# Kernel optimization log

Measured on AMD Instinct MI355X. Metric: run time of the kernel, lower is better.

## Reference

```python
import jax, jax.numpy as jnp
import numpy as np

N_HEADS = 16
D_MODEL = 1024
HEAD_DIM = D_MODEL // N_HEADS
B, S = 2, 2048


def setup_inputs() -> dict:
    key = jax.random.key(0)
    ks = jax.random.split(key, 10)
    scale = 1.0 / np.sqrt(D_MODEL)
    inp = {
        "query_tokens": jax.random.normal(ks[0], (B, S, D_MODEL), dtype=jnp.float32),
        "key_or_value_tokens": jax.random.normal(ks[1], (B, S, D_MODEL), dtype=jnp.float32),
        "mask": jnp.ones((B, S, S), dtype=jnp.int32),
        "Wq": jax.random.normal(ks[2], (D_MODEL, D_MODEL), dtype=jnp.float32) * scale,
        "bq": jnp.zeros((D_MODEL,), dtype=jnp.float32),
        "Wk": jax.random.normal(ks[3], (D_MODEL, D_MODEL), dtype=jnp.float32) * scale,
        "bk": jnp.zeros((D_MODEL,), dtype=jnp.float32),
        "Wv": jax.random.normal(ks[4], (D_MODEL, D_MODEL), dtype=jnp.float32) * scale,
        "bv": jnp.zeros((D_MODEL,), dtype=jnp.float32),
        "Wo": jax.random.normal(ks[5], (D_MODEL, D_MODEL), dtype=jnp.float32) * scale,
        "bo": jnp.zeros((D_MODEL,), dtype=jnp.float32),
    }
    return inp


def reference(query_tokens, key_or_value_tokens, mask, Wq, bq, Wk, bk, Wv, bv, Wo, bo):
    b, s, d = query_tokens.shape
    h, dh = N_HEADS, HEAD_DIM

    def proj(x, W, bias):
        # torch Linear: x @ W.T + b ; then split heads -> (b, h, s, dh)
        y = jnp.einsum("bsd,ed->bse", x, W) + bias
        return y.reshape(b, -1, h, dh).transpose(0, 2, 1, 3)

    q = proj(query_tokens, Wq, bq)
    k = proj(key_or_value_tokens, Wk, bk)
    v = proj(key_or_value_tokens, Wv, bv)

    scores = jnp.einsum("bhqd,bhkd->bhqk", q, k) / jnp.sqrt(jnp.float32(dh))
    # mask: (b, Sq, Sk) -> (b, 1, Sq, Sk); zeros get large negative fill
    scores = jnp.where(mask[:, None, :, :] == 0, jnp.float32(-1e9), scores)
    attn = jax.nn.softmax(scores, axis=-1)
    out = jnp.einsum("bhqk,bhkd->bhqd", attn, v)
    out = out.transpose(0, 2, 1, 3).reshape(b, s, d)
    return jnp.einsum("bsd,ed->bse", out, Wo) + bo
```

## Files before the change

### kernel.cpp

```cpp
#include <hip/hip_runtime.h>
#include <hip/hip_bf16.h>

typedef __bf16 bf16_8 __attribute__((ext_vector_type(8)));
typedef __bf16 bf16_4 __attribute__((ext_vector_type(4)));
typedef float  f32_4  __attribute__((ext_vector_type(4)));

#define NH 16
#define DHD 64
#define BB 2
#define SS 2048
#define DD 1024

__device__ __forceinline__ void gload16(const __bf16* g, __bf16* l) {
    __builtin_amdgcn_global_load_lds(
        (const __attribute__((address_space(1))) void*)g,
        (__attribute__((address_space(3))) void*)l, 16, 0, 0);
}

__global__ __launch_bounds__(256) void conv_all(
    const float* __restrict__ s0, const float* __restrict__ s1,
    const float* __restrict__ s2, const float* __restrict__ s3,
    const float* __restrict__ s4, const float* __restrict__ s5,
    __bf16* __restrict__ d0, __bf16* __restrict__ d1, __bf16* __restrict__ d2,
    __bf16* __restrict__ d3, __bf16* __restrict__ d4, __bf16* __restrict__ d5) {
    const int y = blockIdx.y;
    if (y >= 2 && blockIdx.x >= 1024) return;
    const float* s = (y == 0) ? s0 : (y == 1) ? s1 : (y == 2) ? s2
                   : (y == 3) ? s3 : (y == 4) ? s4 : s5;
    __bf16* d      = (y == 0) ? d0 : (y == 1) ? d1 : (y == 2) ? d2
                   : (y == 3) ? d3 : (y == 4) ? d4 : d5;
    const int i = (blockIdx.x * 256 + threadIdx.x) * 4;
    f32_4 v = *(const f32_4*)&s[i];
    bf16_4 o; o[0] = (__bf16)v[0]; o[1] = (__bf16)v[1];
    o[2] = (__bf16)v[2]; o[3] = (__bf16)v[3];
    *(bf16_4*)&d[i] = o;
}

__global__ __launch_bounds__(256) void mask_flags_k(const int* __restrict__ mask,
                                                    int* __restrict__ flags) {
    const int id = blockIdx.x;
    const int b = id >> 10, qt = (id >> 5) & 31, kt = id & 31;
    const int t = threadIdx.x;
    const int row = t >> 2, seg = t & 3;
    const int* p = mask + ((size_t)b * SS + qt * 64 + row) * SS + kt * 64 + seg * 16;
    int any0 = 0;
#pragma unroll
    for (int i = 0; i < 4; ++i) {
        int4 v = *(const int4*)&p[i * 4];
        any0 |= (v.x == 0) | (v.y == 0) | (v.z == 0) | (v.w == 0);
    }
    unsigned long long bal = __ballot(any0);
    __shared__ int sf[4];
    if ((t & 63) == 0) sf[t >> 6] = (bal != 0ULL);
    __syncthreads();
    if (t == 0) flags[id] = sf[0] | sf[1] | sf[2] | sf[3];
}

template <int LAYOUT>
__device__ __forceinline__ void gemm_body(const __bf16* __restrict__ A,
                                          const __bf16* __restrict__ W,
                                          const float* __restrict__ bias,
                                          __bf16* __restrict__ out,
                                          __bf16* ldsA, __bf16* ldsB) {
    const int tid  = threadIdx.x;
    const int lane = tid & 63;
    const int w    = tid >> 6;
    const int quad = lane >> 4;
    const int l15  = lane & 15;
    const int wm   = (w >> 1) * 64;
    const int wn   = (w & 1) * 64;
    const int m0   = blockIdx.x * 128;
    const int n0   = blockIdx.y * 128;

    f32_4 acc[4][4] = {};

    for (int kt = 0; kt < 1024; kt += 32) {
#pragma unroll
        for (int cc = 0; cc < 2; ++cc) {
            const int c   = tid + cc * 256;
            const int row = c >> 2;
            const int cp  = c & 3;
            gload16(&A[(size_t)(m0 + row) * 1024 + kt + cp * 8], &ldsA[c * 8]);
            gload16(&W[(size_t)(n0 + row) * 1024 + kt + cp * 8], &ldsB[c * 8]);
        }
        __syncthreads();

        bf16_8 af[4], bfr[4];
#pragma unroll
        for (int i = 0; i < 4; ++i)
            af[i] = *(const bf16_8*)&ldsA[(wm + i * 16 + l15) * 32 + quad * 8];
#pragma unroll
        for (int j = 0; j < 4; ++j)
            bfr[j] = *(const bf16_8*)&ldsB[(wn + j * 16 + l15) * 32 + quad * 8];
#pragma unroll
        for (int i = 0; i < 4; ++i)
#pragma unroll
            for (int j = 0; j < 4; ++j)
                acc[i][j] = __builtin_amdgcn_mfma_f32_16x16x32_bf16(
                    af[i], bfr[j], acc[i][j], 0, 0, 0);
        __syncthreads();
    }

#pragma unroll
    for (int i = 0; i < 4; ++i) {
#pragma unroll
        for (int j = 0; j < 4; ++j) {
            const int col = n0 + wn + j * 16 + l15;
            const float bv = bias[col];
            if (LAYOUT == 2) {
                const int row0 = m0 + wm + i * 16 + quad * 4;
                bf16_4 pk;
#pragma unroll
                for (int r = 0; r < 4; ++r) pk[r] = (__bf16)(acc[i][j][r] + bv);
                const int bb = row0 >> 11, s0 = row0 & 2047;
                const int h = col >> 6, dh = col & 63;
                *(bf16_4*)&out[(((size_t)bb * NH + h) * DHD + dh) * SS + s0] = pk;
            } else {
#pragma unroll
                for (int r = 0; r < 4; ++r) {
                    const int row = m0 + wm + i * 16 + quad * 4 + r;
                    out[(((size_t)(row >> 11) * NH + (col >> 6)) * SS +
                         (row & 2047)) * DHD + (col & 63)] =
                        (__bf16)(acc[i][j][r] + bv);
                }
            }
        }
    }
}

__global__ __launch_bounds__(256) void gemm_qkv(
    const __bf16* __restrict__ Xq, const __bf16* __restrict__ Xkv,
    const __bf16* __restrict__ Wq, const float* __restrict__ bq,
    const __bf16* __restrict__ Wk, const float* __restrict__ bk,
    const __bf16* __restrict__ Wv, const float* __restrict__ bv,
    __bf16* __restrict__ Qo, __bf16* __restrict__ Ko, __bf16* __restrict__ VTo) {
    __shared__ __align__(16) __bf16 ldsA[128 * 32];
    __shared__ __align__(16) __bf16 ldsB[128 * 32];
    const int z = blockIdx.z;
    const __bf16* A    = (z == 0) ? Xq : Xkv;
    const __bf16* W    = (z == 0) ? Wq : (z == 1 ? Wk : Wv);
    const float* bias  = (z == 0) ? bq : (z == 1 ? bk : bv);
    if (z == 2)
        gemm_body<2>(A, W, bias, VTo, ldsA, ldsB);
    else
        gemm_body<0>(A, W, bias, (z == 0) ? Qo : Ko, ldsA, ldsB);
}

__global__ __launch_bounds__(256) void gemm_final(
    const __bf16* __restrict__ A, const __bf16* __restrict__ W,
    const float* __restrict__ bias, float* __restrict__ out) {
    __shared__ __align__(16) __bf16 ldsA[64 * 32];
    __shared__ __align__(16) __bf16 ldsB[64 * 32];
    const int tid  = threadIdx.x;
    const int lane = tid & 63;
    const int w    = tid >> 6;
    const int quad = lane >> 4;
    const int l15  = lane & 15;
    const int wm   = (w >> 1) * 32;
    const int wn   = (w & 1) * 32;
    const int m0   = blockIdx.x * 64;
    const int n0   = blockIdx.y * 64;

    const int isB = w >> 1;
    const __bf16* src = isB ? W : A;
    const int     bN  = isB ? n0 : m0;
    __bf16*       dst = isB ? ldsB : ldsA;
    const int     w2  = w & 1;

    f32_4 acc[2][2] = {};

    for (int kt = 0; kt < 1024; kt += 32) {
#pragma unroll
        for (int cc = 0; cc < 2; ++cc) {
            const int c   = w2 * 128 + cc * 64 + lane;
            const int row = c >> 2;
            const int cp  = c & 3;
            gload16(&src[(size_t)(bN + row) * 1024 + kt + cp * 8], &dst[c * 8]);
        }
        __syncthreads();

        bf16_8 af[2], bfr[2];
#pragma unroll
        for (int i = 0; i < 2; ++i)
            af[i] = *(const bf16_8*)&ldsA[(wm + i * 16 + l15) * 32 + quad * 8];
#pragma unroll
        for (int j = 0; j < 2; ++j)
            bfr[j] = *(const bf16_8*)&ldsB[(wn + j * 16 + l15) * 32 + quad * 8];
#pragma unroll
        for (int i = 0; i < 2; ++i)
#pragma unroll
            for (int j = 0; j < 2; ++j)
                acc[i][j] = __builtin_amdgcn_mfma_f32_16x16x32_bf16(
                    af[i], bfr[j], acc[i][j], 0, 0, 0);
        __syncthreads();
    }

#pragma unroll
    for (int i = 0; i < 2; ++i)
#pragma unroll
        for (int j = 0; j < 2; ++j) {
            const int col = n0 + wn + j * 16 + l15;
            const float bv = bias[col];
#pragma unroll
            for (int r = 0; r < 4; ++r) {
                const int row = m0 + wm + i * 16 + quad * 4 + r;
                out[(size_t)row * 1024 + col] = acc[i][j][r] + bv;
            }
        }
}

__global__ __launch_bounds__(256) void flash_attn(
    const __bf16* __restrict__ Q, const __bf16* __restrict__ K,
    const __bf16* __restrict__ VT, const int* __restrict__ mask,
    const int* __restrict__ flags, __bf16* __restrict__ O) {
    __shared__ __align__(16) __bf16 ldsK[64 * 72];
    __shared__ __align__(16) __bf16 ldsVT[64 * 72];
    __shared__ __align__(16) __bf16 ldsP[64 * 72];

    const int tid  = threadIdx.x;
    const int lane = tid & 63;
    const int w    = tid >> 6;
    const int quad = lane >> 4;
    const int l15  = lane & 15;
    const int q0   = blockIdx.x * 64;
    const int bh   = blockIdx.y;
    const int b    = bh >> 4;

    const __bf16* Qb  = Q + (size_t)bh * SS * DHD;
    const __bf16* Kb  = K + (size_t)bh * SS * DHD;
    const __bf16* VTb = VT + (size_t)bh * DHD * SS;
    const int*    mb  = mask + (size_t)b * SS * SS;
    const int*    fl  = flags + ((size_t)b * 32 + blockIdx.x) * 32;

    bf16_8 qa[2];
#pragma unroll
    for (int ks = 0; ks < 2; ++ks) {
        bf16_8 t = *(const bf16_8*)&Qb[(size_t)(q0 + w * 16 + l15) * DHD + ks * 32 + quad * 8];
#pragma unroll
        for (int e = 0; e < 8; ++e)
            qa[ks][e] = (__bf16)((float)t[e] * 0.18033688011112042f);
    }

    f32_4 of[4] = {};
    float li[4] = {0.f, 0.f, 0.f, 0.f};

    const int rowA = tid >> 3,          cpA = tid & 7;
    const int rowB = (tid + 256) >> 3;

    uint4 kr0 = *(const uint4*)&Kb[(size_t)rowA * DHD + cpA * 8];
    uint4 kr1 = *(const uint4*)&Kb[(size_t)rowB * DHD + cpA * 8];
    uint4 vr0 = *(const uint4*)&VTb[(size_t)rowA * SS + cpA * 8];
    uint4 vr1 = *(const uint4*)&VTb[(size_t)rowB * SS + cpA * 8];

    for (int k0 = 0; k0 < SS; k0 += 64) {
        *(uint4*)&ldsK[rowA * 72 + cpA * 8]  = kr0;
        *(uint4*)&ldsK[rowB * 72 + cpA * 8]  = kr1;
        *(uint4*)&ldsVT[rowA * 72 + cpA * 8] = vr0;
        *(uint4*)&ldsVT[rowB * 72 + cpA * 8] = vr1;
        if (k0 + 64 < SS) {
            const int kn = k0 + 64;
            kr0 = *(const uint4*)&Kb[(size_t)(kn + rowA) * DHD + cpA * 8];
            kr1 = *(const uint4*)&Kb[(size_t)(kn + rowB) * DHD + cpA * 8];
            vr0 = *(const uint4*)&VTb[(size_t)rowA * SS + kn + cpA * 8];
            vr1 = *(const uint4*)&VTb[(size_t)rowB * SS + kn + cpA * 8];
        }
        __syncthreads();

        f32_4 sa[4] = {};
#pragma unroll
        for (int ks = 0; ks < 2; ++ks) {
            bf16_8 kb[4];
#pragma unroll
            for (int j = 0; j < 4; ++j)
                kb[j] = *(const bf16_8*)&ldsK[(j * 16 + l15) * 72 + ks * 32 + quad * 8];
#pragma unroll
            for (int j = 0; j < 4; ++j)
                sa[j] = __builtin_amdgcn_mfma_f32_16x16x32_bf16(qa[ks], kb[j], sa[j], 0, 0, 0);
        }

        if (fl[k0 >> 6]) {
#pragma unroll
            for (int j = 0; j < 4; ++j)
#pragma unroll
                for (int r = 0; r < 4; ++r) {
                    const int qg = q0 + w * 16 + quad * 4 + r;
                    const int kg = k0 + j * 16 + l15;
                    if (mb[(size_t)qg * SS + kg] == 0) sa[j][r] = -1e9f;
                }
        }

#pragma unroll
        for (int j = 0; j < 4; ++j)
#pragma unroll
            for (int r = 0; r < 4; ++r) {
                const float p = exp2f(sa[j][r]);
                li[r] += p;
                ldsP[(w * 16 + quad * 4 + r) * 72 + j * 16 + l15] = (__bf16)p;
            }

#pragma unroll
        for (int ks2 = 0; ks2 < 2; ++ks2) {
            bf16_8 pa = *(const bf16_8*)&ldsP[(w * 16 + l15) * 72 + ks2 * 32 + quad * 8];
            bf16_8 vb[4];
#pragma unroll
            for (int jo = 0; jo < 4; ++jo)
                vb[jo] = *(const bf16_8*)&ldsVT[(jo * 16 + l15) * 72 + ks2 * 32 + quad * 8];
#pragma unroll
            for (int jo = 0; jo < 4; ++jo)
                of[jo] = __builtin_amdgcn_mfma_f32_16x16x32_bf16(pa, vb[jo], of[jo], 0, 0, 0);
        }
        __syncthreads();
    }

    const int hcol = (bh & 15) * 64;
#pragma unroll
    for (int r = 0; r < 4; ++r) {
        float ls = li[r];
        ls += __shfl_xor(ls, 1);
        ls += __shfl_xor(ls, 2);
        ls += __shfl_xor(ls, 4);
        ls += __shfl_xor(ls, 8);
        const float inv = 1.0f / fmaxf(ls, 1e-37f);
        const int qg = q0 + w * 16 + quad * 4 + r;
#pragma unroll
        for (int jo = 0; jo < 4; ++jo)
            O[((size_t)b * SS + qg) * DD + hcol + jo * 16 + l15] =
                (__bf16)(of[jo][r] * inv);
    }
}


extern "C" void kernel_launch(void* const* d_in, const int* in_sizes, int n_in,
                              void* d_out, int out_size, void* d_ws, size_t ws_size,
                              hipStream_t stream) {
    const float* xq   = (const float*)d_in[0];
    const float* xkv  = (const float*)d_in[1];
    const int*   mask = (const int*)d_in[2];
    const float* Wq   = (const float*)d_in[3];
    const float* bq   = (const float*)d_in[4];
    const float* Wk   = (const float*)d_in[5];
    const float* bk   = (const float*)d_in[6];
    const float* Wv   = (const float*)d_in[7];
    const float* bv   = (const float*)d_in[8];
    const float* Wo   = (const float*)d_in[9];
    const float* bo   = (const float*)d_in[10];

    __bf16* ws = (__bf16*)d_ws;
    const size_t big = (size_t)BB * SS * DD;
    const size_t wsz = (size_t)DD * DD;
    __bf16* Qw   = ws;
    __bf16* Kw   = Qw + big;
    __bf16* VTw  = Kw + big;
    __bf16* Aw   = VTw + big;
    __bf16* Xqb  = Aw + big;
    __bf16* Xkvb = Xqb + big;
    __bf16* Wqb  = Xkvb + big;
    __bf16* Wkb  = Wqb + wsz;
    __bf16* Wvb  = Wkb + wsz;
    __bf16* Wob  = Wvb + wsz;
    int* flags   = (int*)(Wob + wsz);

    dim3 blk(256);
    conv_all<<<dim3(4096, 6), blk, 0, stream>>>(xq, xkv, Wq, Wk, Wv, Wo,
                                                Xqb, Xkvb, Wqb, Wkb, Wvb, Wob);
    mask_flags_k<<<dim3(2048), blk, 0, stream>>>(mask, flags);
    gemm_qkv<<<dim3(32, 8, 3), blk, 0, stream>>>(Xqb, Xkvb, Wqb, bq, Wkb, bk,
                                                 Wvb, bv, Qw, Kw, VTw);
    flash_attn<<<dim3(SS / 64, BB * NH), blk, 0, stream>>>(Qw, Kw, VTw, mask,
                                                           flags, Aw);
    gemm_final<<<dim3(64, 16), blk, 0, stream>>>(Aw, Wob, bo, (float*)d_out);
}
```

Measured before the change: 274.0 us.

## Switch flash attention to 32x32x16 MFMA with two-wave blocks and shared K/P LDS

Rewrites the attention kernel so each of two waves owns 32 query rows and uses 32x32x16 bf16 MFMA for both QK^T and PV, instead of four waves each doing 16-row 16x16x32 tiles. The K tile buffer is reused to hold the P tile after an extra barrier, which cuts LDS use, and launch bounds become 128 threads with a min-blocks hint of 3. The aim is fewer MFMA and LDS-read instructions per tile and more resident blocks. The cost is an extra __syncthreads per iteration, more accumulator registers per thread, and half as many threads per block to hide load latency.

```diff
diff --git a/kernel.cpp b/kernel.cpp
--- a/kernel.cpp
+++ b/kernel.cpp
@@ -1,9 +1,11 @@
 #include <hip/hip_runtime.h>
 #include <hip/hip_bf16.h>
 
-typedef __bf16 bf16_8 __attribute__((ext_vector_type(8)));
-typedef __bf16 bf16_4 __attribute__((ext_vector_type(4)));
-typedef float  f32_4  __attribute__((ext_vector_type(4)));
+typedef __bf16 bf16_8  __attribute__((ext_vector_type(8)));
+typedef __bf16 bf16_4  __attribute__((ext_vector_type(4)));
+typedef __bf16 bf16_16 __attribute__((ext_vector_type(16)));
+typedef float  f32_4   __attribute__((ext_vector_type(4)));
+typedef float  f32_16  __attribute__((ext_vector_type(16)));
 
 #define NH 16
 #define DHD 64
@@ -209,19 +211,18 @@
         }
 }
 
-__global__ __launch_bounds__(256) void flash_attn(
+__global__ __launch_bounds__(128, 3) void flash_attn(
     const __bf16* __restrict__ Q, const __bf16* __restrict__ K,
     const __bf16* __restrict__ VT, const int* __restrict__ mask,
     const int* __restrict__ flags, __bf16* __restrict__ O) {
-    __shared__ __align__(16) __bf16 ldsK[64 * 72];
+    __shared__ __align__(16) __bf16 ldsKP[64 * 72];
     __shared__ __align__(16) __bf16 ldsVT[64 * 72];
-    __shared__ __align__(16) __bf16 ldsP[64 * 72];
 
     const int tid  = threadIdx.x;
     const int lane = tid & 63;
     const int w    = tid >> 6;
-    const int quad = lane >> 4;
-    const int l15  = lane & 15;
+    const int l31  = lane & 31;
+    const int hl   = lane >> 5;
     const int q0   = blockIdx.x * 64;
     const int bh   = blockIdx.y;
     const int b    = bh >> 4;
@@ -232,100 +233,110 @@
     const int*    mb  = mask + (size_t)b * SS * SS;
     const int*    fl  = flags + ((size_t)b * 32 + blockIdx.x) * 32;
 
-    bf16_8 qa[2];
-#pragma unroll
-    for (int ks = 0; ks < 2; ++ks) {
-        bf16_8 t = *(const bf16_8*)&Qb[(size_t)(q0 + w * 16 + l15) * DHD + ks * 32 + quad * 8];
+    bf16_8 qa[4];
+#pragma unroll
+    for (int ks = 0; ks < 4; ++ks) {
+        bf16_8 t = *(const bf16_8*)&Qb[(size_t)(q0 + w * 32 + l31) * DHD +
+                                       ks * 16 + hl * 8];
 #pragma unroll
         for (int e = 0; e < 8; ++e)
             qa[ks][e] = (__bf16)((float)t[e] * 0.18033688011112042f);
     }
 
-    f32_4 of[4] = {};
-    float li[4] = {0.f, 0.f, 0.f, 0.f};
-
-    const int rowA = tid >> 3,          cpA = tid & 7;
-    const int rowB = (tid + 256) >> 3;
-
-    uint4 kr0 = *(const uint4*)&Kb[(size_t)rowA * DHD + cpA * 8];
-    uint4 kr1 = *(const uint4*)&Kb[(size_t)rowB * DHD + cpA * 8];
-    uint4 vr0 = *(const uint4*)&VTb[(size_t)rowA * SS + cpA * 8];
-    uint4 vr1 = *(const uint4*)&VTb[(size_t)rowB * SS + cpA * 8];
+    f32_16 of0 = {}, of1 = {};
+    float li[16];
+#pragma unroll
+    for (int r = 0; r < 16; ++r) li[r] = 0.f;
+
+    const int rK = tid >> 3;
+    const int cp = tid & 7;
+    uint4 pre[8];
+#pragma unroll
+    for (int i = 0; i < 4; ++i) {
+        pre[i]     = *(const uint4*)&Kb[(size_t)(rK + i * 16) * DHD + cp * 8];
+        pre[4 + i] = *(const uint4*)&VTb[(size_t)(rK + i * 16) * SS + cp * 8];
+    }
 
     for (int k0 = 0; k0 < SS; k0 += 64) {
-        *(uint4*)&ldsK[rowA * 72 + cpA * 8]  = kr0;
-        *(uint4*)&ldsK[rowB * 72 + cpA * 8]  = kr1;
-        *(uint4*)&ldsVT[rowA * 72 + cpA * 8] = vr0;
-        *(uint4*)&ldsVT[rowB * 72 + cpA * 8] = vr1;
+#pragma unroll
+        for (int i = 0; i < 4; ++i) {
+            *(uint4*)&ldsKP[(rK + i * 16) * 72 + cp * 8] = pre[i];
+            *(uint4*)&ldsVT[(rK + i * 16) * 72 + cp * 8] = pre[4 + i];
+        }
         if (k0 + 64 < SS) {
             const int kn = k0 + 64;
-            kr0 = *(const uint4*)&Kb[(size_t)(kn + rowA) * DHD + cpA * 8];
-            kr1 = *(const uint4*)&Kb[(size_t)(kn + rowB) * DHD + cpA * 8];
-            vr0 = *(const uint4*)&VTb[(size_t)rowA * SS + kn + cpA * 8];
-            vr1 = *(const uint4*)&VTb[(size_t)rowB * SS + kn + cpA * 8];
-        }
-        __syncthreads();
-
-        f32_4 sa[4] = {};
-#pragma unroll
-        for (int ks = 0; ks < 2; ++ks) {
-            bf16_8 kb[4];
-#pragma unroll
-            for (int j = 0; j < 4; ++j)
-                kb[j] = *(const bf16_8*)&ldsK[(j * 16 + l15) * 72 + ks * 32 + quad * 8];
-#pragma unroll
-            for (int j = 0; j < 4; ++j)
-                sa[j] = __builtin_amdgcn_mfma_f32_16x16x32_bf16(qa[ks], kb[j], sa[j], 0, 0, 0);
-        }
-
-        if (fl[k0 >> 6]) {
-#pragma unroll
-            for (int j = 0; j < 4; ++j)
-#pragma unroll
-                for (int r = 0; r < 4; ++r) {
-                    const int qg = q0 + w * 16 + quad * 4 + r;
-                    const int kg = k0 + j * 16 + l15;
-                    if (mb[(size_t)qg * SS + kg] == 0) sa[j][r] = -1e9f;
+#pragma unroll
+            for (int i = 0; i < 4; ++i) {
+                pre[i]     = *(const uint4*)&Kb[(size_t)(kn + rK + i * 16) * DHD + cp * 8];
+                pre[4 + i] = *(const uint4*)&VTb[(size_t)(rK + i * 16) * SS + kn + cp * 8];
+            }
+        }
+        __syncthreads();
+
+        const bool msk = (fl[k0 >> 6] != 0);
+        bf16_16 p16[2];
+
+#pragma unroll
+        for (int jt = 0; jt < 2; ++jt) {
+            f32_16 s = {};
+#pragma unroll
+            for (int ks = 0; ks < 4; ++ks) {
+                bf16_8 kb = *(const bf16_8*)&ldsKP[(jt * 32 + l31) * 72 +
+                                                   ks * 16 + hl * 8];
+                s = __builtin_amdgcn_mfma_f32_32x32x16_bf16(qa[ks], kb, s, 0, 0, 0);
+            }
+            if (msk) {
+#pragma unroll
+                for (int r = 0; r < 16; ++r) {
+                    const int row = (r & 3) + 8 * (r >> 2) + 4 * hl;
+                    const int qg  = q0 + w * 32 + row;
+                    const int kg  = k0 + jt * 32 + l31;
+                    if (mb[(size_t)qg * SS + kg] == 0) s[r] = -1e9f;
                 }
-        }
-
-#pragma unroll
-        for (int j = 0; j < 4; ++j)
-#pragma unroll
-            for (int r = 0; r < 4; ++r) {
-                const float p = exp2f(sa[j][r]);
+            }
+#pragma unroll
+            for (int r = 0; r < 16; ++r) {
+                const float p = exp2f(s[r]);
                 li[r] += p;
-                ldsP[(w * 16 + quad * 4 + r) * 72 + j * 16 + l15] = (__bf16)p;
-            }
-
-#pragma unroll
-        for (int ks2 = 0; ks2 < 2; ++ks2) {
-            bf16_8 pa = *(const bf16_8*)&ldsP[(w * 16 + l15) * 72 + ks2 * 32 + quad * 8];
-            bf16_8 vb[4];
-#pragma unroll
-            for (int jo = 0; jo < 4; ++jo)
-                vb[jo] = *(const bf16_8*)&ldsVT[(jo * 16 + l15) * 72 + ks2 * 32 + quad * 8];
-#pragma unroll
-            for (int jo = 0; jo < 4; ++jo)
-                of[jo] = __builtin_amdgcn_mfma_f32_16x16x32_bf16(pa, vb[jo], of[jo], 0, 0, 0);
+                p16[jt][r] = (__bf16)p;
+            }
+        }
+        __syncthreads();
+
+#pragma unroll
+        for (int jt = 0; jt < 2; ++jt)
+#pragma unroll
+            for (int r = 0; r < 16; ++r) {
+                const int row = (r & 3) + 8 * (r >> 2) + 4 * hl;
+                ldsKP[(w * 32 + row) * 72 + jt * 32 + l31] = p16[jt][r];
+            }
+
+#pragma unroll
+        for (int ks2 = 0; ks2 < 4; ++ks2) {
+            bf16_8 pa = *(const bf16_8*)&ldsKP[(w * 32 + l31) * 72 +
+                                               ks2 * 16 + hl * 8];
+            bf16_8 vb0 = *(const bf16_8*)&ldsVT[(l31) * 72 + ks2 * 16 + hl * 8];
+            bf16_8 vb1 = *(const bf16_8*)&ldsVT[(32 + l31) * 72 + ks2 * 16 + hl * 8];
+            of0 = __builtin_amdgcn_mfma_f32_32x32x16_bf16(pa, vb0, of0, 0, 0, 0);
+            of1 = __builtin_amdgcn_mfma_f32_32x32x16_bf16(pa, vb1, of1, 0, 0, 0);
         }
         __syncthreads();
     }
 
     const int hcol = (bh & 15) * 64;
 #pragma unroll
-    for (int r = 0; r < 4; ++r) {
+    for (int r = 0; r < 16; ++r) {
         float ls = li[r];
         ls += __shfl_xor(ls, 1);
         ls += __shfl_xor(ls, 2);
         ls += __shfl_xor(ls, 4);
         ls += __shfl_xor(ls, 8);
+        ls += __shfl_xor(ls, 16);
         const float inv = 1.0f / fmaxf(ls, 1e-37f);
-        const int qg = q0 + w * 16 + quad * 4 + r;
-#pragma unroll
-        for (int jo = 0; jo < 4; ++jo)
-            O[((size_t)b * SS + qg) * DD + hcol + jo * 16 + l15] =
-                (__bf16)(of[jo][r] * inv);
+        const int row = (r & 3) + 8 * (r >> 2) + 4 * hl;
+        const int qg  = q0 + w * 32 + row;
+        O[((size_t)b * SS + qg) * DD + hcol + l31]      = (__bf16)(of0[r] * inv);
+        O[((size_t)b * SS + qg) * DD + hcol + 32 + l31] = (__bf16)(of1[r] * inv);
     }
 }
 
@@ -360,13 +371,12 @@
     __bf16* Wob  = Wvb + wsz;
     int* flags   = (int*)(Wob + wsz);
 
-    dim3 blk(256);
-    conv_all<<<dim3(4096, 6), blk, 0, stream>>>(xq, xkv, Wq, Wk, Wv, Wo,
-                                                Xqb, Xkvb, Wqb, Wkb, Wvb, Wob);
-    mask_flags_k<<<dim3(2048), blk, 0, stream>>>(mask, flags);
-    gemm_qkv<<<dim3(32, 8, 3), blk, 0, stream>>>(Xqb, Xkvb, Wqb, bq, Wkb, bk,
-                                                 Wvb, bv, Qw, Kw, VTw);
-    flash_attn<<<dim3(SS / 64, BB * NH), blk, 0, stream>>>(Qw, Kw, VTw, mask,
-                                                           flags, Aw);
-    gemm_final<<<dim3(64, 16), blk, 0, stream>>>(Aw, Wob, bo, (float*)d_out);
-}
+    conv_all<<<dim3(4096, 6), dim3(256), 0, stream>>>(xq, xkv, Wq, Wk, Wv, Wo,
+                                                      Xqb, Xkvb, Wqb, Wkb, Wvb, Wob);
+    mask_flags_k<<<dim3(2048), dim3(256), 0, stream>>>(mask, flags);
+    gemm_qkv<<<dim3(32, 8, 3), dim3(256), 0, stream>>>(Xqb, Xkvb, Wqb, bq, Wkb, bk,
+                                                       Wvb, bv, Qw, Kw, VTw);
+    flash_attn<<<dim3(SS / 64, BB * NH), dim3(128), 0, stream>>>(Qw, Kw, VTw, mask,
+                                                                 flags, Aw);
+    gemm_final<<<dim3(64, 16), dim3(256), 0, stream>>>(Aw, Wob, bo, (float*)d_out);
+}
```

Result: slower. 404.7 us (+47.7%).

## Double flash-attention query tile to 128 rows per block for K/V reuse

Applied to the files above, without the earlier changes.

Each attention block now covers 128 query rows instead of 64, with each wave handling two 16-row MFMA tiles. The goal is to reuse every K/V tile loaded into LDS across twice as many queries, halving global K/V traffic and the number of staging loads. It adds a __syncthreads between the P write and the P·V read, doubles the P buffer, halves the grid to 512 blocks, and raises register pressure; launch bounds ask for 2 blocks per CU. The mask check now ORs flags for two 64-row query groups.

```diff
diff --git a/kernel.cpp b/kernel.cpp
--- a/kernel.cpp
+++ b/kernel.cpp
@@ -1,9 +1,9 @@
 #include <hip/hip_runtime.h>
 #include <hip/hip_bf16.h>
 
-typedef __bf16 bf16_8 __attribute__((ext_vector_type(8)));
-typedef __bf16 bf16_4 __attribute__((ext_vector_type(4)));
-typedef float  f32_4  __attribute__((ext_vector_type(4)));
+typedef __bf16 bf16_8  __attribute__((ext_vector_type(8)));
+typedef __bf16 bf16_4  __attribute__((ext_vector_type(4)));
+typedef float  f32_4   __attribute__((ext_vector_type(4)));
 
 #define NH 16
 #define DHD 64
@@ -209,20 +209,20 @@
         }
 }
 
-__global__ __launch_bounds__(256) void flash_attn(
+__global__ __launch_bounds__(256, 2) void flash_attn(
     const __bf16* __restrict__ Q, const __bf16* __restrict__ K,
     const __bf16* __restrict__ VT, const int* __restrict__ mask,
     const int* __restrict__ flags, __bf16* __restrict__ O) {
     __shared__ __align__(16) __bf16 ldsK[64 * 72];
     __shared__ __align__(16) __bf16 ldsVT[64 * 72];
-    __shared__ __align__(16) __bf16 ldsP[64 * 72];
+    __shared__ __align__(16) __bf16 ldsP[128 * 72];
 
     const int tid  = threadIdx.x;
     const int lane = tid & 63;
     const int w    = tid >> 6;
     const int quad = lane >> 4;
     const int l15  = lane & 15;
-    const int q0   = blockIdx.x * 64;
+    const int q0   = blockIdx.x * 128;
     const int bh   = blockIdx.y;
     const int b    = bh >> 4;
 
@@ -230,43 +230,48 @@
     const __bf16* Kb  = K + (size_t)bh * SS * DHD;
     const __bf16* VTb = VT + (size_t)bh * DHD * SS;
     const int*    mb  = mask + (size_t)b * SS * SS;
-    const int*    fl  = flags + ((size_t)b * 32 + blockIdx.x) * 32;
-
-    bf16_8 qa[2];
-#pragma unroll
-    for (int ks = 0; ks < 2; ++ks) {
-        bf16_8 t = *(const bf16_8*)&Qb[(size_t)(q0 + w * 16 + l15) * DHD + ks * 32 + quad * 8];
-#pragma unroll
-        for (int e = 0; e < 8; ++e)
-            qa[ks][e] = (__bf16)((float)t[e] * 0.18033688011112042f);
-    }
-
-    f32_4 of[4] = {};
-    float li[4] = {0.f, 0.f, 0.f, 0.f};
-
-    const int rowA = tid >> 3,          cpA = tid & 7;
-    const int rowB = (tid + 256) >> 3;
-
-    uint4 kr0 = *(const uint4*)&Kb[(size_t)rowA * DHD + cpA * 8];
-    uint4 kr1 = *(const uint4*)&Kb[(size_t)rowB * DHD + cpA * 8];
-    uint4 vr0 = *(const uint4*)&VTb[(size_t)rowA * SS + cpA * 8];
-    uint4 vr1 = *(const uint4*)&VTb[(size_t)rowB * SS + cpA * 8];
+    const int*    flb = flags + (size_t)b * 1024 + blockIdx.x * 64;
+
+    bf16_8 qa[2][2];
+#pragma unroll
+    for (int mt = 0; mt < 2; ++mt)
+#pragma unroll
+        for (int ks = 0; ks < 2; ++ks) {
+            bf16_8 t = *(const bf16_8*)&Qb[(size_t)(q0 + w * 32 + mt * 16 + l15) * DHD +
+                                           ks * 32 + quad * 8];
+#pragma unroll
+            for (int e = 0; e < 8; ++e)
+                qa[mt][ks][e] = (__bf16)((float)t[e] * 0.18033688011112042f);
+        }
+
+    f32_4 of[2][4] = {};
+    float li[2][4] = {};
+
+    const int r0 = tid >> 3;
+    const int r1 = r0 + 32;
+    const int cp = tid & 7;
+    uint4 kr0 = *(const uint4*)&Kb[(size_t)r0 * DHD + cp * 8];
+    uint4 kr1 = *(const uint4*)&Kb[(size_t)r1 * DHD + cp * 8];
+    uint4 vr0 = *(const uint4*)&VTb[(size_t)r0 * SS + cp * 8];
+    uint4 vr1 = *(const uint4*)&VTb[(size_t)r1 * SS + cp * 8];
 
     for (int k0 = 0; k0 < SS; k0 += 64) {
-        *(uint4*)&ldsK[rowA * 72 + cpA * 8]  = kr0;
-        *(uint4*)&ldsK[rowB * 72 + cpA * 8]  = kr1;
-        *(uint4*)&ldsVT[rowA * 72 + cpA * 8] = vr0;
-        *(uint4*)&ldsVT[rowB * 72 + cpA * 8] = vr1;
+        *(uint4*)&ldsK[r0 * 72 + cp * 8]  = kr0;
+        *(uint4*)&ldsK[r1 * 72 + cp * 8]  = kr1;
+        *(uint4*)&ldsVT[r0 * 72 + cp * 8] = vr0;
+        *(uint4*)&ldsVT[r1 * 72 + cp * 8] = vr1;
         if (k0 + 64 < SS) {
             const int kn = k0 + 64;
-            kr0 = *(const uint4*)&Kb[(size_t)(kn + rowA) * DHD + cpA * 8];
-            kr1 = *(const uint4*)&Kb[(size_t)(kn + rowB) * DHD + cpA * 8];
-            vr0 = *(const uint4*)&VTb[(size_t)rowA * SS + kn + cpA * 8];
-            vr1 = *(const uint4*)&VTb[(size_t)rowB * SS + kn + cpA * 8];
-        }
-        __syncthreads();
-
-        f32_4 sa[4] = {};
+            kr0 = *(const uint4*)&Kb[(size_t)(kn + r0) * DHD + cp * 8];
+            kr1 = *(const uint4*)&Kb[(size_t)(kn + r1) * DHD + cp * 8];
+            vr0 = *(const uint4*)&VTb[(size_t)r0 * SS + kn + cp * 8];
+            vr1 = *(const uint4*)&VTb[(size_t)r1 * SS + kn + cp * 8];
+        }
+        __syncthreads();
+
+        const bool msk = ((flb[k0 >> 6] | flb[32 + (k0 >> 6)]) != 0);
+
+        f32_4 sa[2][4] = {};
 #pragma unroll
         for (int ks = 0; ks < 2; ++ks) {
             bf16_8 kb[4];
@@ -274,59 +279,77 @@
             for (int j = 0; j < 4; ++j)
                 kb[j] = *(const bf16_8*)&ldsK[(j * 16 + l15) * 72 + ks * 32 + quad * 8];
 #pragma unroll
+            for (int mt = 0; mt < 2; ++mt)
+#pragma unroll
+                for (int j = 0; j < 4; ++j)
+                    sa[mt][j] = __builtin_amdgcn_mfma_f32_16x16x32_bf16(
+                        qa[mt][ks], kb[j], sa[mt][j], 0, 0, 0);
+        }
+
+        if (msk) {
+#pragma unroll
+            for (int mt = 0; mt < 2; ++mt)
+#pragma unroll
+                for (int j = 0; j < 4; ++j)
+#pragma unroll
+                    for (int r = 0; r < 4; ++r) {
+                        const int qg = q0 + w * 32 + mt * 16 + quad * 4 + r;
+                        const int kg = k0 + j * 16 + l15;
+                        if (mb[(size_t)qg * SS + kg] == 0) sa[mt][j][r] = -1e9f;
+                    }
+        }
+
+#pragma unroll
+        for (int mt = 0; mt < 2; ++mt)
+#pragma unroll
             for (int j = 0; j < 4; ++j)
-                sa[j] = __builtin_amdgcn_mfma_f32_16x16x32_bf16(qa[ks], kb[j], sa[j], 0, 0, 0);
-        }
-
-        if (fl[k0 >> 6]) {
-#pragma unroll
-            for (int j = 0; j < 4; ++j)
 #pragma unroll
                 for (int r = 0; r < 4; ++r) {
-                    const int qg = q0 + w * 16 + quad * 4 + r;
-                    const int kg = k0 + j * 16 + l15;
-                    if (mb[(size_t)qg * SS + kg] == 0) sa[j][r] = -1e9f;
+                    const float p = exp2f(sa[mt][j][r]);
+                    li[mt][r] += p;
+                    ldsP[(w * 32 + mt * 16 + quad * 4 + r) * 72 + j * 16 + l15] =
+                        (__bf16)p;
                 }
-        }
-
-#pragma unroll
-        for (int j = 0; j < 4; ++j)
-#pragma unroll
-            for (int r = 0; r < 4; ++r) {
-                const float p = exp2f(sa[j][r]);
-                li[r] += p;
-                ldsP[(w * 16 + quad * 4 + r) * 72 + j * 16 + l15] = (__bf16)p;
-            }
+        __syncthreads();
 
 #pragma unroll
         for (int ks2 = 0; ks2 < 2; ++ks2) {
-            bf16_8 pa = *(const bf16_8*)&ldsP[(w * 16 + l15) * 72 + ks2 * 32 + quad * 8];
-            bf16_8 vb[4];
+            bf16_8 pa[2], vb[4];
+#pragma unroll
+            for (int mt = 0; mt < 2; ++mt)
+                pa[mt] = *(const bf16_8*)&ldsP[(w * 32 + mt * 16 + l15) * 72 +
+                                               ks2 * 32 + quad * 8];
 #pragma unroll
             for (int jo = 0; jo < 4; ++jo)
-                vb[jo] = *(const bf16_8*)&ldsVT[(jo * 16 + l15) * 72 + ks2 * 32 + quad * 8];
+                vb[jo] = *(const bf16_8*)&ldsVT[(jo * 16 + l15) * 72 +
+                                                ks2 * 32 + quad * 8];
+#pragma unroll
+            for (int mt = 0; mt < 2; ++mt)
+#pragma unroll
+                for (int jo = 0; jo < 4; ++jo)
+                    of[mt][jo] = __builtin_amdgcn_mfma_f32_16x16x32_bf16(
+                        pa[mt], vb[jo], of[mt][jo], 0, 0, 0);
+        }
+        __syncthreads();
+    }
+
+    const int hcol = (bh & 15) * 64;
+#pragma unroll
+    for (int mt = 0; mt < 2; ++mt)
+#pragma unroll
+        for (int r = 0; r < 4; ++r) {
+            float ls = li[mt][r];
+            ls += __shfl_xor(ls, 1);
+            ls += __shfl_xor(ls, 2);
+            ls += __shfl_xor(ls, 4);
+            ls += __shfl_xor(ls, 8);
+            const float inv = 1.0f / fmaxf(ls, 1e-37f);
+            const int qg = q0 + w * 32 + mt * 16 + quad * 4 + r;
 #pragma unroll
             for (int jo = 0; jo < 4; ++jo)
-                of[jo] = __builtin_amdgcn_mfma_f32_16x16x32_bf16(pa, vb[jo], of[jo], 0, 0, 0);
-        }
-        __syncthreads();
-    }
-
-    const int hcol = (bh & 15) * 64;
-#pragma unroll
-    for (int r = 0; r < 4; ++r) {
-        float ls = li[r];
-        ls += __shfl_xor(ls, 1);
-        ls += __shfl_xor(ls, 2);
-        ls += __shfl_xor(ls, 4);
-        ls += __shfl_xor(ls, 8);
-        const float inv = 1.0f / fmaxf(ls, 1e-37f);
-        const int qg = q0 + w * 16 + quad * 4 + r;
-#pragma unroll
-        for (int jo = 0; jo < 4; ++jo)
-            O[((size_t)b * SS + qg) * DD + hcol + jo * 16 + l15] =
-                (__bf16)(of[jo][r] * inv);
-    }
+                O[((size_t)b * SS + qg) * DD + hcol + jo * 16 + l15] =
+                    (__bf16)(of[mt][jo][r] * inv);
+        }
 }
 
 
@@ -360,13 +383,12 @@
     __bf16* Wob  = Wvb + wsz;
     int* flags   = (int*)(Wob + wsz);
 
-    dim3 blk(256);
-    conv_all<<<dim3(4096, 6), blk, 0, stream>>>(xq, xkv, Wq, Wk, Wv, Wo,
-                                                Xqb, Xkvb, Wqb, Wkb, Wvb, Wob);
-    mask_flags_k<<<dim3(2048), blk, 0, stream>>>(mask, flags);
-    gemm_qkv<<<dim3(32, 8, 3), blk, 0, stream>>>(Xqb, Xkvb, Wqb, bq, Wkb, bk,
-                                                 Wvb, bv, Qw, Kw, VTw);
-    flash_attn<<<dim3(SS / 64, BB * NH), blk, 0, stream>>>(Qw, Kw, VTw, mask,
-                                                           flags, Aw);
-    gemm_final<<<dim3(64, 16), blk, 0, stream>>>(Aw, Wob, bo, (float*)d_out);
-}
+    conv_all<<<dim3(4096, 6), dim3(256), 0, stream>>>(xq, xkv, Wq, Wk, Wv, Wo,
+                                                      Xqb, Xkvb, Wqb, Wkb, Wvb, Wob);
+    mask_flags_k<<<dim3(2048), dim3(256), 0, stream>>>(mask, flags);
+    gemm_qkv<<<dim3(32, 8, 3), dim3(256), 0, stream>>>(Xqb, Xkvb, Wqb, bq, Wkb, bk,
+                                                       Wvb, bv, Qw, Kw, VTw);
+    flash_attn<<<dim3(SS / 128, BB * NH), dim3(256), 0, stream>>>(Qw, Kw, VTw, mask,
+                                                                  flags, Aw);
+    gemm_final<<<dim3(64, 16), dim3(256), 0, stream>>>(Aw, Wob, bo, (float*)d_out);
+}
```

Result: faster. 268.1 us (-2.1%).
